# Kernel tuning notes

Measured on AMD Instinct MI355X. Metric: run time of the kernel, lower is better.

## Reference

```python
import jax, jax.numpy as jnp
import numpy as np

H, HKV, D, HID, INT = 16, 4, 128, 2048, 8192
ROPE_THETA = 10000.0
EPS = 1e-6
NEG = -1e30


def rmsnorm(x, w):
    v = jnp.mean(x * x, axis=-1, keepdims=True)
    return x * jax.lax.rsqrt(v + EPS) * w


def apply_rope(t, pos):
    # t: [B,S,h,D], pos: [S]
    half = D // 2
    inv_freq = 1.0 / (ROPE_THETA ** (jnp.arange(0, half, dtype=jnp.float32) / half))
    ang = pos.astype(jnp.float32)[:, None] * inv_freq  # [S, D/2]
    cos = jnp.cos(ang)[None, :, None, :]
    sin = jnp.sin(ang)[None, :, None, :]
    t1, t2 = t[..., :half], t[..., half:]
    return jnp.concatenate([t1 * cos - t2 * sin, t2 * cos + t1 * sin], axis=-1)


def setup_inputs() -> dict:
    key = jax.random.key(0)
    ks = jax.random.split(key, 5)
    B, S = 4, 1024
    s = 0.02  # init scale for weights
    return {
        "x": jax.random.normal(ks[0], (B, S, HID), jnp.float32),
        "ln1_w": jnp.ones((HID,), jnp.float32),
        "wqkv": jax.random.normal(ks[1], (HID, (H + 2 * HKV) * D), jnp.float32) * s,
        "wo": jax.random.normal(ks[2], (H * D, HID), jnp.float32) * s,
        "ln2_w": jnp.ones((HID,), jnp.float32),
        "w_gate_up": jax.random.normal(ks[3], (HID, 2 * INT), jnp.float32) * s,
        "w_down": jax.random.normal(ks[4], (INT, HID), jnp.float32) * s,
        "pos": jnp.arange(S, dtype=jnp.int32),
    }


def reference(x, ln1_w, wqkv, wo, ln2_w, w_gate_up, w_down, pos):
    B, S, _ = x.shape
    # --- attention block (prefill paged attention == dense causal attention) ---
    h = rmsnorm(x, ln1_w)
    qkv = h @ wqkv  # [B,S,(H+2*HKV)*D]
    q = qkv[..., : H * D].reshape(B, S, H, D)
    k = qkv[..., H * D : (H + HKV) * D].reshape(B, S, HKV, D)
    v = qkv[..., (H + HKV) * D :].reshape(B, S, HKV, D)
    q = apply_rope(q, pos)
    k = apply_rope(k, pos)
    g = H // HKV  # GQA group size
    k = jnp.repeat(k, g, axis=2)
    v = jnp.repeat(v, g, axis=2)
    scores = jnp.einsum("bqhd,bkhd->bhqk", q, k) / np.float32(np.sqrt(D))
    causal = pos[:, None] >= pos[None, :]  # [S,S]
    scores = jnp.where(causal[None, None], scores, NEG)
    attn = jax.nn.softmax(scores, axis=-1)
    o = jnp.einsum("bhqk,bkhd->bqhd", attn, v).reshape(B, S, H * D) @ wo
    h1 = x + o
    # --- SwiGLU MLP block ---
    gu = rmsnorm(h1, ln2_w) @ w_gate_up
    gate, up = gu[..., :INT], gu[..., INT:]
    return h1 + (jax.nn.silu(gate) * up) @ w_down
```

## Files before the change

kernel.cpp:

```cpp
#include <hip/hip_runtime.h>
#include <math.h>

#define B_    4
#define S_    1024
#define H_    16
#define HKV_  4
#define D_    128
#define HID_  2048
#define INT_  8192
#define QKVD_ 3072
#define NTOK_ 4096
#define NEG_  -1.0e30f

typedef unsigned short u16;
typedef unsigned int   u32;
typedef float  f32x4  __attribute__((ext_vector_type(4)));
typedef __bf16 bf16x8 __attribute__((ext_vector_type(8)));

__device__ __forceinline__ float bf2f(u16 v) {
    union { u32 u; float f; } c; c.u = ((u32)v) << 16; return c.f;
}
__device__ __forceinline__ u16 f2bf(float f) {
    union { float f; u32 u; } c; c.f = f;
    return (u16)((c.u + 0x7fffu + ((c.u >> 16) & 1u)) >> 16);
}

__device__ __forceinline__ void async_ld16(const u16* g, u16* l) {
    __builtin_amdgcn_global_load_lds(
        (const __attribute__((address_space(1))) void*)g,
        (__attribute__((address_space(3))) void*)l, 16, 0, 0);
}

__global__ void detect_k(const u16* __restrict__ w, int* __restrict__ flag) {
    if (threadIdx.x == 0) *flag = (w[0] == 0x3F80u) ? 0 : 1;
}

__global__ void cvt_x_k(const void* __restrict__ in, const int* __restrict__ flag,
                        u16* __restrict__ out) {
    int i = blockIdx.x * 256 + threadIdx.x;
    if (*flag == 0) {
        ((ushort4*)out)[i] = ((const ushort4*)in)[i];
    } else {
        float4 v = ((const float4*)in)[i];
        ushort4 o;
        o.x = f2bf(v.x); o.y = f2bf(v.y); o.z = f2bf(v.z); o.w = f2bf(v.w);
        ((ushort4*)out)[i] = o;
    }
}

__global__ void cvt_w_k(const void* __restrict__ in, const int* __restrict__ flag,
                        float* __restrict__ out, int n) {
    int i = blockIdx.x * 256 + threadIdx.x;
    if (i < n) out[i] = (*flag == 0) ? bf2f(((const u16*)in)[i]) : ((const float*)in)[i];
}

__global__ void transpose_k(const void* __restrict__ in, const int* __restrict__ flag,
                            u16* __restrict__ out, int K, int N) {
    __shared__ u16 t[64][65];
    const bool isf32 = (*flag != 0);
    int tx = blockIdx.x * 64;
    int ty = blockIdx.y * 64;
    const int c4 = (threadIdx.x & 15) * 4;
    const int r0 = threadIdx.x >> 4;
    for (int r = r0; r < 64; r += 16) {
        size_t idx = (size_t)(ty + r) * N + tx + c4;
        if (isf32) {
            float4 v = *(const float4*)((const float*)in + idx);
            t[c4 + 0][r] = f2bf(v.x); t[c4 + 1][r] = f2bf(v.y);
            t[c4 + 2][r] = f2bf(v.z); t[c4 + 3][r] = f2bf(v.w);
        } else {
            ushort4 v = *(const ushort4*)((const u16*)in + idx);
            t[c4 + 0][r] = v.x; t[c4 + 1][r] = v.y;
            t[c4 + 2][r] = v.z; t[c4 + 3][r] = v.w;
        }
    }
    __syncthreads();
    for (int i = threadIdx.x; i < 64 * 16; i += 256) {
        int r = i >> 4, c = (i & 15) * 4;
        ushort4 v;
        v.x = t[r][c]; v.y = t[r][c + 1]; v.z = t[r][c + 2]; v.w = t[r][c + 3];
        *(ushort4*)(out + (size_t)(tx + r) * K + ty + c) = v;
    }
}

__global__ void rmsnorm_k(const u16* __restrict__ x, const float* __restrict__ w,
                          u16* __restrict__ y) {
    int row = blockIdx.x;
    const u16* xr = x + (size_t)row * HID_;
    u16* yr = y + (size_t)row * HID_;
    int t = threadIdx.x;
    u16 xs[8];
    *(uint4*)xs = ((const uint4*)xr)[t];
    float v[8]; float ss = 0.f;
    #pragma unroll
    for (int i = 0; i < 8; i++) { v[i] = bf2f(xs[i]); ss += v[i] * v[i]; }
    #pragma unroll
    for (int o = 32; o > 0; o >>= 1) ss += __shfl_down(ss, o, 64);
    __shared__ float wsum[4];
    if ((t & 63) == 0) wsum[t >> 6] = ss;
    __syncthreads();
    float tot = wsum[0] + wsum[1] + wsum[2] + wsum[3];
    float scale = rsqrtf(tot * (1.0f / HID_) + 1e-6f);
    float4 w0 = ((const float4*)w)[t * 2];
    float4 w1 = ((const float4*)w)[t * 2 + 1];
    float wf[8] = {w0.x, w0.y, w0.z, w0.w, w1.x, w1.y, w1.z, w1.w};
    u16 ys[8];
    #pragma unroll
    for (int i = 0; i < 8; i++) ys[i] = f2bf(v[i] * scale * wf[i]);
    ((uint4*)yr)[t] = *(uint4*)ys;
}

__global__ void rope_table_k(const int* __restrict__ pos,
                             float* __restrict__ cosT, float* __restrict__ sinT) {
    int s = blockIdx.x;
    int d = threadIdx.x;
    double inv = exp(-((double)d / 64.0) * 9.210340371976184);
    double ang = (double)pos[s] * inv;
    cosT[s * 64 + d] = (float)cos(ang);
    sinT[s * 64 + d] = (float)sin(ang);
}

__global__ void rope_apply_k(u16* __restrict__ qkv, const float* __restrict__ cosT,
                             const float* __restrict__ sinT) {
    int id = blockIdx.x * 256 + threadIdx.x;
    int d4 = (id & 15) * 4;
    int rest = id >> 4;
    int head = rest % 20;
    int bs = rest / 20;
    int s = bs & (S_ - 1);
    size_t base = (size_t)bs * QKVD_ + head * D_;
    ushort4 lo = *(ushort4*)(qkv + base + d4);
    ushort4 hi = *(ushort4*)(qkv + base + 64 + d4);
    float4 c  = *(const float4*)(cosT + s * 64 + d4);
    float4 sn = *(const float4*)(sinT + s * 64 + d4);
    float t1[4] = {bf2f(lo.x), bf2f(lo.y), bf2f(lo.z), bf2f(lo.w)};
    float t2[4] = {bf2f(hi.x), bf2f(hi.y), bf2f(hi.z), bf2f(hi.w)};
    float cf[4] = {c.x, c.y, c.z, c.w};
    float sf[4] = {sn.x, sn.y, sn.z, sn.w};
    ushort4 olo, ohi;
    olo.x = f2bf(t1[0] * cf[0] - t2[0] * sf[0]);
    olo.y = f2bf(t1[1] * cf[1] - t2[1] * sf[1]);
    olo.z = f2bf(t1[2] * cf[2] - t2[2] * sf[2]);
    olo.w = f2bf(t1[3] * cf[3] - t2[3] * sf[3]);
    ohi.x = f2bf(t2[0] * cf[0] + t1[0] * sf[0]);
    ohi.y = f2bf(t2[1] * cf[1] + t1[1] * sf[1]);
    ohi.z = f2bf(t2[2] * cf[2] + t1[2] * sf[2]);
    ohi.w = f2bf(t2[3] * cf[3] + t1[3] * sf[3]);
    *(ushort4*)(qkv + base + d4)      = olo;
    *(ushort4*)(qkv + base + 64 + d4) = ohi;
}

template<int EPI>
__global__ __launch_bounds__(256) void gemm_bt_k(
    const u16* __restrict__ A, const u16* __restrict__ Bt,
    void* __restrict__ Cv, const u16* __restrict__ R,
    const int* __restrict__ flag, int M, int N, int K)
{
    __shared__ __align__(16) u16 As[128 * 32];
    __shared__ __align__(16) u16 Bs[128 * 32];

    int bx = blockIdx.x, by = blockIdx.y;
    {
        const int gx  = gridDim.x;
        const int nwg = gx * gridDim.y;
        const int orig = by * gx + bx;
        const int q = nwg >> 3, r = nwg & 7;
        const int xcd = orig & 7, loc = orig >> 3;
        const int wg = (xcd < r ? xcd * (q + 1) : r * (q + 1) + (xcd - r) * q) + loc;
        bx = wg % gx; by = wg / gx;
    }

    const int tid  = threadIdx.x;
    const int m0 = by * 128;
    const int n0 = bx * 128;
    const int wave = tid >> 6, lane = tid & 63;
    const int wm = (wave & 1) * 64, wn = (wave >> 1) * 64;
    const int r16 = lane & 15, quad = lane >> 4;

    const int f0 = tid * 8;
    const int f1 = f0 + 2048;
    const size_t arow0 = (size_t)(m0 + (f0 >> 5)) * K + (f0 & 31);
    const size_t arow1 = (size_t)(m0 + (f1 >> 5)) * K + (f1 & 31);
    const size_t brow0 = (size_t)(n0 + (f0 >> 5)) * K + (f0 & 31);
    const size_t brow1 = (size_t)(n0 + (f1 >> 5)) * K + (f1 & 31);

    f32x4 acc[4][4] = {};

    for (int k0 = 0; k0 < K; k0 += 32) {
        async_ld16(A  + arow0 + k0, As + f0);
        async_ld16(A  + arow1 + k0, As + f1);
        async_ld16(Bt + brow0 + k0, Bs + f0);
        async_ld16(Bt + brow1 + k0, Bs + f1);
        __syncthreads();
        bf16x8 a[4], b[4];
        #pragma unroll
        for (int i = 0; i < 4; i++)
            a[i] = *(const bf16x8*)(As + (wm + i * 16 + r16) * 32 + quad * 8);
        #pragma unroll
        for (int j = 0; j < 4; j++)
            b[j] = *(const bf16x8*)(Bs + (wn + j * 16 + r16) * 32 + quad * 8);
        #pragma unroll
        for (int i = 0; i < 4; i++)
            #pragma unroll
            for (int j = 0; j < 4; j++)
                acc[i][j] = __builtin_amdgcn_mfma_f32_16x16x32_bf16(a[i], b[j], acc[i][j], 0, 0, 0);
        __syncthreads();
    }

    u16* C16 = (u16*)Cv;
    float* C32 = (float*)Cv;
    bool f32out = false;
    if (EPI == 3) f32out = (*flag != 0);

    #pragma unroll
    for (int i = 0; i < 4; i++) {
        const int mb = m0 + wm + i * 16 + quad * 4;
        #pragma unroll
        for (int j = 0; j < 4; j++) {
            const int n = n0 + wn + j * 16 + r16;
            #pragma unroll
            for (int r = 0; r < 4; r++) {
                size_t idx = (size_t)(mb + r) * N + n;
                float v = acc[i][j][r];
                if (EPI == 1 || EPI == 3) v += bf2f(R[idx]);
                if (EPI == 3 && f32out) C32[idx] = v;
                else C16[idx] = f2bf(v);
            }
        }
    }
}

template<int EPI>
__global__ __launch_bounds__(512, 2) void gemm256_k(
    const u16* __restrict__ A, const u16* __restrict__ Bt,
    void* __restrict__ Cv, int M, int N, int K)
{
    __shared__ __align__(16) u16 lds[3 * 16384];

    int bx = blockIdx.x, by = blockIdx.y;
    {
        const int gx  = gridDim.x;
        const int nwg = gx * gridDim.y;
        const int orig = by * gx + bx;
        const int q = nwg >> 3, r = nwg & 7;
        const int xcd = orig & 7, loc = orig >> 3;
        const int wg = (xcd < r ? xcd * (q + 1) : r * (q + 1) + (xcd - r) * q) + loc;
        bx = wg % gx; by = wg / gx;
    }

    const int tid  = threadIdx.x;
    const int m0 = by * 256, n0 = bx * 256;
    const int wave = tid >> 6, lane = tid & 63;
    const int wmi = wave >> 2, wni = wave & 3;
    const int r16 = lane & 15, quad = lane >> 4;

    const int NT = K >> 5;

    auto stageA = [&](int bufi, int tt) {
        u16* dst = lds + bufi * 16384;
        const size_t gb = (size_t)m0 * K + (size_t)tt * 32;
        #pragma unroll
        for (int rr = 0; rr < 2; ++rr) {
            const int e = rr * 4096 + tid * 8;
            async_ld16(A + gb + (size_t)(e >> 5) * K + (e & 31), dst + e);
        }
    };
    auto stageB = [&](int bufi, int tt) {
        u16* dst = lds + bufi * 16384 + 8192;
        const size_t gb = (size_t)n0 * K + (size_t)tt * 32;
        #pragma unroll
        for (int rr = 0; rr < 2; ++rr) {
            const int e = rr * 4096 + tid * 8;
            async_ld16(Bt + gb + (size_t)(e >> 5) * K + (e & 31), dst + e);
        }
    };

    f32x4 acc[8][4] = {};

    stageA(0, 0); stageB(0, 0);
    stageA(1, 1); stageB(1, 1);
    asm volatile("s_waitcnt vmcnt(4)" ::: "memory");
    __builtin_amdgcn_s_barrier();

    const int aoff = wmi * 4096 + r16 * 32 + quad * 8;
    const int boff = 8192 + wni * 2048 + r16 * 32 + quad * 8;

    for (int t = 0; t < NT; ++t) {
        const u16* buf = lds + (t % 3) * 16384;
        const int nb = (t + 2) % 3;
        const bool pf = (t + 2) < NT;
        bf16x8 a[4], b[4], a2[4];
        #pragma unroll
        for (int i = 0; i < 4; ++i) a[i] = *(const bf16x8*)(buf + aoff + i * 512);
        #pragma unroll
        for (int j = 0; j < 4; ++j) b[j] = *(const bf16x8*)(buf + boff + j * 512);
        if (pf) stageA(nb, t + 2);
        __builtin_amdgcn_s_barrier();
        asm volatile("s_waitcnt lgkmcnt(0)" ::: "memory");
        __builtin_amdgcn_sched_barrier(0);
        __builtin_amdgcn_s_setprio(1);
        #pragma unroll
        for (int i = 0; i < 4; ++i)
            #pragma unroll
            for (int j = 0; j < 4; ++j)
                acc[i][j] = __builtin_amdgcn_mfma_f32_16x16x32_bf16(a[i], b[j], acc[i][j], 0, 0, 0);
        __builtin_amdgcn_s_setprio(0);
        __builtin_amdgcn_s_barrier();
        #pragma unroll
        for (int i = 0; i < 4; ++i) a2[i] = *(const bf16x8*)(buf + aoff + (i + 4) * 512);
        if (pf) stageB(nb, t + 2);
        __builtin_amdgcn_s_barrier();
        asm volatile("s_waitcnt lgkmcnt(0)" ::: "memory");
        __builtin_amdgcn_sched_barrier(0);
        __builtin_amdgcn_s_setprio(1);
        #pragma unroll
        for (int i = 0; i < 4; ++i)
            #pragma unroll
            for (int j = 0; j < 4; ++j)
                acc[i + 4][j] = __builtin_amdgcn_mfma_f32_16x16x32_bf16(a2[i], b[j], acc[i + 4][j], 0, 0, 0);
        __builtin_amdgcn_s_setprio(0);
        if (t == NT - 2) { asm volatile("s_waitcnt vmcnt(0)" ::: "memory"); }
        else             { asm volatile("s_waitcnt vmcnt(4)" ::: "memory"); }
        __builtin_amdgcn_s_barrier();
    }

    u16* C16 = (u16*)Cv;
    #pragma unroll
    for (int i = 0; i < 8; ++i) {
        const int mb = m0 + wmi * 128 + i * 16 + quad * 4;
        #pragma unroll
        for (int j = 0; j < 4; ++j) {
            const int n = n0 + wni * 64 + j * 16 + r16;
            #pragma unroll
            for (int r = 0; r < 4; ++r) {
                size_t idx = (size_t)(mb + r) * N + n;
                float v = acc[i][j][r];
                if (EPI == 2) { v = v / (1.f + __expf(-v)); v *= bf2f(C16[idx]); }
                C16[idx] = f2bf(v);
            }
        }
    }
}

__global__ __launch_bounds__(256) void attn_mfma_k(
    const u16* __restrict__ qkv, u16* __restrict__ out)
{
    __shared__ __align__(16) u16 Vt[128 * 136];
    __shared__ __align__(16) u16 Ps[64 * 136];

    int bswz_x, bswz_y, bswz_z;
    {
        const int orig = blockIdx.x + (S_ / 64) * (blockIdx.y + H_ * blockIdx.z);
        const int q = ((S_ / 64) * H_ * B_) >> 3;
        const int wg = (orig & 7) * q + (orig >> 3);
        bswz_x = wg & (S_ / 64 - 1);
        bswz_y = (wg >> 4) & (H_ - 1);
        bswz_z = wg >> 8;
    }

    const int tid  = threadIdx.x;
    const int wave = tid >> 6, lane = tid & 63;
    const int r16  = lane & 15, quad = lane >> 4;
    const int q0 = bswz_x * 64;
    const int h  = bswz_y;
    const int b  = bswz_z;
    const int kh = h >> 2;
    const float scale = 0.08838834764831845f;

    bf16x8 a_q[4];
    {
        const u16* qp = qkv + ((size_t)(b * S_ + q0 + wave * 16 + r16) * QKVD_ + h * D_ + quad * 8);
        #pragma unroll
        for (int ks = 0; ks < 4; ks++)
            a_q[ks] = *(const bf16x8*)(qp + ks * 32);
    }

    float mrun[4], lrun[4];
    #pragma unroll
    for (int r = 0; r < 4; r++) { mrun[r] = -3.0e38f; lrun[r] = 0.f; }
    f32x4 acc_o[8] = {};
    const int myrow_c = q0 + wave * 16 + quad * 4;

    const int ntiles = (q0 >> 7) + 1;
    for (int kt = 0; kt < ntiles; kt++) {
        const int j0 = kt * 128;
        __syncthreads();
        {
            const int key = tid & 127, dh = (tid >> 7) * 64;
            const u16* vp = qkv + ((size_t)(b * S_ + j0 + key) * QKVD_ + (H_ + HKV_ + kh) * D_ + dh);
            #pragma unroll
            for (int i = 0; i < 8; i++) {
                u16 tmp[8];
                *(uint4*)tmp = *(const uint4*)(vp + i * 8);
                #pragma unroll
                for (int j = 0; j < 8; j++)
                    Vt[(dh + i * 8 + j) * 136 + key] = tmp[j];
            }
        }
        f32x4 acc_s[8] = {};
        __builtin_amdgcn_s_setprio(1);
        #pragma unroll
        for (int ks = 0; ks < 4; ks++) {
            #pragma unroll
            for (int nt = 0; nt < 8; nt++) {
                const u16* kp = qkv + ((size_t)(b * S_ + j0 + nt * 16 + r16) * QKVD_
                                       + (H_ + kh) * D_ + ks * 32 + quad * 8);
                bf16x8 bk = *(const bf16x8*)kp;
                acc_s[nt] = __builtin_amdgcn_mfma_f32_16x16x32_bf16(a_q[ks], bk, acc_s[nt], 0, 0, 0);
            }
        }
        __builtin_amdgcn_s_setprio(0);
        const bool lastt = (kt == ntiles - 1);
        float mnew[4];
        #pragma unroll
        for (int r = 0; r < 4; r++) mnew[r] = mrun[r];
        #pragma unroll
        for (int nt = 0; nt < 8; nt++) {
            const int col = j0 + nt * 16 + r16;
            #pragma unroll
            for (int r = 0; r < 4; r++) {
                float v = acc_s[nt][r] * scale;
                if (lastt && col > myrow_c + r) v = NEG_;
                acc_s[nt][r] = v;
                mnew[r] = fmaxf(mnew[r], v);
            }
        }
        #pragma unroll
        for (int o = 1; o < 16; o <<= 1)
            #pragma unroll
            for (int r = 0; r < 4; r++)
                mnew[r] = fmaxf(mnew[r], __shfl_xor(mnew[r], o, 64));
        float alpha[4], lsum[4];
        #pragma unroll
        for (int r = 0; r < 4; r++) {
            alpha[r] = __expf(mrun[r] - mnew[r]);
            mrun[r] = mnew[r];
            lsum[r] = 0.f;
        }
        #pragma unroll
        for (int nt = 0; nt < 8; nt++) {
            #pragma unroll
            for (int r = 0; r < 4; r++) {
                float p = __expf(acc_s[nt][r] - mrun[r]);
                lsum[r] += p;
                Ps[(wave * 16 + quad * 4 + r) * 136 + nt * 16 + r16] = f2bf(p);
            }
        }
        #pragma unroll
        for (int o = 1; o < 16; o <<= 1)
            #pragma unroll
            for (int r = 0; r < 4; r++)
                lsum[r] += __shfl_xor(lsum[r], o, 64);
        #pragma unroll
        for (int r = 0; r < 4; r++) lrun[r] = lrun[r] * alpha[r] + lsum[r];
        #pragma unroll
        for (int nt = 0; nt < 8; nt++)
            #pragma unroll
            for (int r = 0; r < 4; r++) acc_o[nt][r] *= alpha[r];
        __syncthreads();
        __builtin_amdgcn_s_setprio(1);
        #pragma unroll
        for (int ks = 0; ks < 4; ks++) {
            bf16x8 ap = *(const bf16x8*)(Ps + (wave * 16 + r16) * 136 + ks * 32 + quad * 8);
            #pragma unroll
            for (int nt = 0; nt < 8; nt++) {
                bf16x8 bv = *(const bf16x8*)(Vt + (nt * 16 + r16) * 136 + ks * 32 + quad * 8);
                acc_o[nt] = __builtin_amdgcn_mfma_f32_16x16x32_bf16(ap, bv, acc_o[nt], 0, 0, 0);
            }
        }
        __builtin_amdgcn_s_setprio(0);
    }
    #pragma unroll
    for (int r = 0; r < 4; r++) {
        const float linv = 1.0f / lrun[r];
        const int tok = myrow_c + r;
        u16* orow = out + ((size_t)(b * S_ + tok) * (H_ * D_) + h * D_ + r16);
        #pragma unroll
        for (int nt = 0; nt < 8; nt++)
            orow[nt * 16] = f2bf(acc_o[nt][r] * linv);
    }
}

extern "C" void kernel_launch(void* const* d_in, const int* in_sizes, int n_in,
                              void* d_out, int out_size, void* d_ws, size_t ws_size,
                              hipStream_t stream)
{
    const void* x    = d_in[0];
    const u16*  ln1w = (const u16*)d_in[1];
    const void* wqkv = d_in[2];
    const void* wo   = d_in[3];
    const void* ln2w = d_in[4];
    const void* wgu  = d_in[5];
    const void* wd   = d_in[6];
    const int*  pos  = (const int*)d_in[7];

    char* wsb = (char*)d_ws;
    size_t off = 0;
    auto alloc = [&](size_t bytes) {
        char* p = wsb + off; off = (off + bytes + 255) & ~(size_t)255; return p;
    };
    int*  flag  = (int*)alloc(256);
    u16*  xb    = (u16*)alloc(2ull * NTOK_ * HID_);
    float* wln1 = (float*)alloc(4ull * HID_);
    float* wln2 = (float*)alloc(4ull * HID_);
    u16* wqkvT = (u16*)alloc(2ull * 3072 * 2048);
    u16* woT   = (u16*)alloc(2ull * 2048 * 2048);
    u16* wguT  = (u16*)alloc(2ull * 16384 * 2048);
    u16* wdT   = (u16*)alloc(2ull * 2048 * 8192);
    u16* h     = (u16*)alloc(2ull * NTOK_ * HID_);
    u16* qkv   = (u16*)alloc(2ull * NTOK_ * QKVD_);
    u16* h1    = (u16*)alloc(2ull * NTOK_ * HID_);
    u16* su    = (u16*)alloc(2ull * NTOK_ * INT_);
    float* cosT = (float*)alloc(4ull * S_ * 64);
    float* sinT = (float*)alloc(4ull * S_ * 64);
    u16* attn_out = h;
    u16* mlp_in   = qkv;

    detect_k<<<1, 64, 0, stream>>>(ln1w, flag);

    cvt_x_k<<<(NTOK_ * HID_ / 4 + 255) / 256, 256, 0, stream>>>(x, flag, xb);
    cvt_w_k<<<8, 256, 0, stream>>>(d_in[1], flag, wln1, HID_);
    cvt_w_k<<<8, 256, 0, stream>>>(ln2w, flag, wln2, HID_);

    transpose_k<<<dim3(3072 / 64, 2048 / 64), 256, 0, stream>>>(wqkv, flag, wqkvT, 2048, 3072);
    transpose_k<<<dim3(2048 / 64, 2048 / 64), 256, 0, stream>>>(wo, flag, woT, 2048, 2048);
    transpose_k<<<dim3(16384 / 64, 2048 / 64), 256, 0, stream>>>(wgu, flag, wguT, 2048, 16384);
    transpose_k<<<dim3(2048 / 64, 8192 / 64), 256, 0, stream>>>(wd, flag, wdT, 8192, 2048);

    rope_table_k<<<S_, 64, 0, stream>>>(pos, cosT, sinT);

    rmsnorm_k<<<NTOK_, 256, 0, stream>>>(xb, wln1, h);
    gemm256_k<0><<<dim3(3072 / 256, NTOK_ / 256), 512, 0, stream>>>(
        h, wqkvT, qkv, NTOK_, QKVD_, HID_);
    rope_apply_k<<<(NTOK_ * 20 * 16) / 256, 256, 0, stream>>>(qkv, cosT, sinT);
    attn_mfma_k<<<dim3(S_ / 64, H_, B_), 256, 0, stream>>>(qkv, attn_out);
    gemm_bt_k<1><<<dim3(2048 / 128, NTOK_ / 128), 256, 0, stream>>>(
        attn_out, woT, h1, xb, nullptr, NTOK_, HID_, HID_);
    rmsnorm_k<<<NTOK_, 256, 0, stream>>>(h1, wln2, mlp_in);
    gemm256_k<0><<<dim3(8192 / 256, NTOK_ / 256), 512, 0, stream>>>(
        mlp_in, wguT + (size_t)8192 * 2048, su, NTOK_, INT_, HID_);
    gemm256_k<2><<<dim3(8192 / 256, NTOK_ / 256), 512, 0, stream>>>(
        mlp_in, wguT, su, NTOK_, INT_, HID_);
    gemm_bt_k<3><<<dim3(2048 / 128, NTOK_ / 128), 256, 0, stream>>>(
        su, wdT, d_out, h1, flag, NTOK_, HID_, INT_);
}
```

Measured before the change: 1.150 ms.

## Replace residual GEMMs with pipelined 128x256 kernel and swizzle LDS tiles

The simple 128x128 gemm_bt_k used for the o-projection and down-projection becomes gemm_bt2_k, a 512-thread kernel with 128x256 tiles and a triple-buffered async-LDS pipeline modeled on gemm256_k. An XOR swizzle of the global column offset, matched by a permuted read offset, is added to both GEMMs to reduce LDS bank conflicts on the fragment reads. The aim is better latency hiding and higher MFMA use on the K=2048 and K=8192 residual GEMMs. The cost is a smaller grid (256 blocks for N=2048) and tighter register and LDS budgets, and the swizzle must index correctly.

```diff
diff --git a/kernel.cpp b/kernel.cpp
--- a/kernel.cpp
+++ b/kernel.cpp
@@ -29,6 +29,10 @@
     __builtin_amdgcn_global_load_lds(
         (const __attribute__((address_space(1))) void*)g,
         (__attribute__((address_space(3))) void*)l, 16, 0, 0);
+}
+
+__device__ __forceinline__ int swz_col(int e) {
+    return ((((e >> 3) & 3) ^ ((e >> 5) & 3) ^ ((e >> 7) & 3)) << 3);
 }
 
 __global__ void detect_k(const u16* __restrict__ w, int* __restrict__ flag) {
@@ -151,13 +155,11 @@
 }
 
 template<int EPI>
-__global__ __launch_bounds__(256) void gemm_bt_k(
+__global__ __launch_bounds__(512, 2) void gemm256_k(
     const u16* __restrict__ A, const u16* __restrict__ Bt,
-    void* __restrict__ Cv, const u16* __restrict__ R,
-    const int* __restrict__ flag, int M, int N, int K)
+    void* __restrict__ Cv, int M, int N, int K)
 {
-    __shared__ __align__(16) u16 As[128 * 32];
-    __shared__ __align__(16) u16 Bs[128 * 32];
+    __shared__ __align__(16) u16 lds[3 * 16384];
 
     int bx = blockIdx.x, by = blockIdx.y;
     {
@@ -171,71 +173,107 @@
     }
 
     const int tid  = threadIdx.x;
-    const int m0 = by * 128;
-    const int n0 = bx * 128;
+    const int m0 = by * 256, n0 = bx * 256;
     const int wave = tid >> 6, lane = tid & 63;
-    const int wm = (wave & 1) * 64, wn = (wave >> 1) * 64;
+    const int wmi = wave >> 2, wni = wave & 3;
     const int r16 = lane & 15, quad = lane >> 4;
 
-    const int f0 = tid * 8;
-    const int f1 = f0 + 2048;
-    const size_t arow0 = (size_t)(m0 + (f0 >> 5)) * K + (f0 & 31);
-    const size_t arow1 = (size_t)(m0 + (f1 >> 5)) * K + (f1 & 31);
-    const size_t brow0 = (size_t)(n0 + (f0 >> 5)) * K + (f0 & 31);
-    const size_t brow1 = (size_t)(n0 + (f1 >> 5)) * K + (f1 & 31);
-
-    f32x4 acc[4][4] = {};
-
-    for (int k0 = 0; k0 < K; k0 += 32) {
-        async_ld16(A  + arow0 + k0, As + f0);
-        async_ld16(A  + arow1 + k0, As + f1);
-        async_ld16(Bt + brow0 + k0, Bs + f0);
-        async_ld16(Bt + brow1 + k0, Bs + f1);
-        __syncthreads();
-        bf16x8 a[4], b[4];
-        #pragma unroll
-        for (int i = 0; i < 4; i++)
-            a[i] = *(const bf16x8*)(As + (wm + i * 16 + r16) * 32 + quad * 8);
-        #pragma unroll
-        for (int j = 0; j < 4; j++)
-            b[j] = *(const bf16x8*)(Bs + (wn + j * 16 + r16) * 32 + quad * 8);
-        #pragma unroll
-        for (int i = 0; i < 4; i++)
-            #pragma unroll
-            for (int j = 0; j < 4; j++)
+    const int NT = K >> 5;
+
+    auto stageA = [&](int bufi, int tt) {
+        u16* dst = lds + bufi * 16384;
+        const size_t gb = (size_t)m0 * K + (size_t)tt * 32;
+        #pragma unroll
+        for (int rr = 0; rr < 2; ++rr) {
+            const int e = rr * 4096 + tid * 8;
+            async_ld16(A + gb + (size_t)(e >> 5) * K + swz_col(e), dst + e);
+        }
+    };
+    auto stageB = [&](int bufi, int tt) {
+        u16* dst = lds + bufi * 16384 + 8192;
+        const size_t gb = (size_t)n0 * K + (size_t)tt * 32;
+        #pragma unroll
+        for (int rr = 0; rr < 2; ++rr) {
+            const int e = rr * 4096 + tid * 8;
+            async_ld16(Bt + gb + (size_t)(e >> 5) * K + swz_col(e), dst + e);
+        }
+    };
+
+    f32x4 acc[8][4] = {};
+
+    stageA(0, 0); stageB(0, 0);
+    stageA(1, 1); stageB(1, 1);
+    asm volatile("s_waitcnt vmcnt(4)" ::: "memory");
+    __builtin_amdgcn_s_barrier();
+
+    const int gsw = quad ^ (r16 & 3) ^ ((r16 >> 2) & 3);
+    const int aoff = wmi * 4096 + r16 * 32 + gsw * 8;
+    const int boff = 8192 + wni * 2048 + r16 * 32 + gsw * 8;
+
+    for (int t = 0; t < NT; ++t) {
+        const u16* buf = lds + (t % 3) * 16384;
+        const int nb = (t + 2) % 3;
+        const bool pf = (t + 2) < NT;
+        bf16x8 a[4], b[4], a2[4];
+        #pragma unroll
+        for (int i = 0; i < 4; ++i) a[i] = *(const bf16x8*)(buf + aoff + i * 512);
+        #pragma unroll
+        for (int j = 0; j < 4; ++j) b[j] = *(const bf16x8*)(buf + boff + j * 512);
+        if (pf) stageA(nb, t + 2);
+        __builtin_amdgcn_s_barrier();
+        asm volatile("s_waitcnt lgkmcnt(0)" ::: "memory");
+        __builtin_amdgcn_sched_barrier(0);
+        __builtin_amdgcn_s_setprio(1);
+        #pragma unroll
+        for (int i = 0; i < 4; ++i)
+            #pragma unroll
+            for (int j = 0; j < 4; ++j)
                 acc[i][j] = __builtin_amdgcn_mfma_f32_16x16x32_bf16(a[i], b[j], acc[i][j], 0, 0, 0);
-        __syncthreads();
+        __builtin_amdgcn_s_setprio(0);
+        __builtin_amdgcn_s_barrier();
+        #pragma unroll
+        for (int i = 0; i < 4; ++i) a2[i] = *(const bf16x8*)(buf + aoff + (i + 4) * 512);
+        if (pf) stageB(nb, t + 2);
+        __builtin_amdgcn_s_barrier();
+        asm volatile("s_waitcnt lgkmcnt(0)" ::: "memory");
+        __builtin_amdgcn_sched_barrier(0);
+        __builtin_amdgcn_s_setprio(1);
+        #pragma unroll
+        for (int i = 0; i < 4; ++i)
+            #pragma unroll
+            for (int j = 0; j < 4; ++j)
+                acc[i + 4][j] = __builtin_amdgcn_mfma_f32_16x16x32_bf16(a2[i], b[j], acc[i + 4][j], 0, 0, 0);
+        __builtin_amdgcn_s_setprio(0);
+        if (t == NT - 2) { asm volatile("s_waitcnt vmcnt(0)" ::: "memory"); }
+        else             { asm volatile("s_waitcnt vmcnt(4)" ::: "memory"); }
+        __builtin_amdgcn_s_barrier();
     }
 
     u16* C16 = (u16*)Cv;
-    float* C32 = (float*)Cv;
-    bool f32out = false;
-    if (EPI == 3) f32out = (*flag != 0);
-
-    #pragma unroll
-    for (int i = 0; i < 4; i++) {
-        const int mb = m0 + wm + i * 16 + quad * 4;
-        #pragma unroll
-        for (int j = 0; j < 4; j++) {
-            const int n = n0 + wn + j * 16 + r16;
-            #pragma unroll
-            for (int r = 0; r < 4; r++) {
+    #pragma unroll
+    for (int i = 0; i < 8; ++i) {
+        const int mb = m0 + wmi * 128 + i * 16 + quad * 4;
+        #pragma unroll
+        for (int j = 0; j < 4; ++j) {
+            const int n = n0 + wni * 64 + j * 16 + r16;
+            #pragma unroll
+            for (int r = 0; r < 4; ++r) {
                 size_t idx = (size_t)(mb + r) * N + n;
                 float v = acc[i][j][r];
-                if (EPI == 1 || EPI == 3) v += bf2f(R[idx]);
-                if (EPI == 3 && f32out) C32[idx] = v;
-                else C16[idx] = f2bf(v);
+                if (EPI == 2) { v = v / (1.f + __expf(-v)); v *= bf2f(C16[idx]); }
+                C16[idx] = f2bf(v);
             }
         }
     }
 }
 
 template<int EPI>
-__global__ __launch_bounds__(512, 2) void gemm256_k(
+__global__ __launch_bounds__(512, 2) void gemm_bt2_k(
     const u16* __restrict__ A, const u16* __restrict__ Bt,
-    void* __restrict__ Cv, int M, int N, int K)
+    void* __restrict__ Cv, const u16* __restrict__ R,
+    const int* __restrict__ flag, int M, int N, int K)
 {
-    __shared__ __align__(16) u16 lds[3 * 16384];
+    __shared__ __align__(16) u16 lds[3 * 12288];
 
     int bx = blockIdx.x, by = blockIdx.y;
     {
@@ -249,7 +287,7 @@
     }
 
     const int tid  = threadIdx.x;
-    const int m0 = by * 256, n0 = bx * 256;
+    const int m0 = by * 128, n0 = bx * 256;
     const int wave = tid >> 6, lane = tid & 63;
     const int wmi = wave >> 2, wni = wave & 3;
     const int r16 = lane & 15, quad = lane >> 4;
@@ -257,43 +295,41 @@
     const int NT = K >> 5;
 
     auto stageA = [&](int bufi, int tt) {
-        u16* dst = lds + bufi * 16384;
+        u16* dst = lds + bufi * 12288;
         const size_t gb = (size_t)m0 * K + (size_t)tt * 32;
+        const int e = tid * 8;
+        async_ld16(A + gb + (size_t)(e >> 5) * K + swz_col(e), dst + e);
+    };
+    auto stageB = [&](int bufi, int tt) {
+        u16* dst = lds + bufi * 12288 + 4096;
+        const size_t gb = (size_t)n0 * K + (size_t)tt * 32;
         #pragma unroll
         for (int rr = 0; rr < 2; ++rr) {
             const int e = rr * 4096 + tid * 8;
-            async_ld16(A + gb + (size_t)(e >> 5) * K + (e & 31), dst + e);
+            async_ld16(Bt + gb + (size_t)(e >> 5) * K + swz_col(e), dst + e);
         }
     };
-    auto stageB = [&](int bufi, int tt) {
-        u16* dst = lds + bufi * 16384 + 8192;
-        const size_t gb = (size_t)n0 * K + (size_t)tt * 32;
-        #pragma unroll
-        for (int rr = 0; rr < 2; ++rr) {
-            const int e = rr * 4096 + tid * 8;
-            async_ld16(Bt + gb + (size_t)(e >> 5) * K + (e & 31), dst + e);
-        }
-    };
-
-    f32x4 acc[8][4] = {};
+
+    f32x4 acc[4][4] = {};
 
     stageA(0, 0); stageB(0, 0);
     stageA(1, 1); stageB(1, 1);
-    asm volatile("s_waitcnt vmcnt(4)" ::: "memory");
+    asm volatile("s_waitcnt vmcnt(3)" ::: "memory");
     __builtin_amdgcn_s_barrier();
 
-    const int aoff = wmi * 4096 + r16 * 32 + quad * 8;
-    const int boff = 8192 + wni * 2048 + r16 * 32 + quad * 8;
+    const int gsw = quad ^ (r16 & 3) ^ ((r16 >> 2) & 3);
+    const int aoff = wmi * 2048 + r16 * 32 + gsw * 8;
+    const int boff = 4096 + wni * 2048 + r16 * 32 + gsw * 8;
 
     for (int t = 0; t < NT; ++t) {
-        const u16* buf = lds + (t % 3) * 16384;
+        const u16* buf = lds + (t % 3) * 12288;
         const int nb = (t + 2) % 3;
         const bool pf = (t + 2) < NT;
-        bf16x8 a[4], b[4], a2[4];
+        bf16x8 a[4], b2[2], b3[2];
         #pragma unroll
         for (int i = 0; i < 4; ++i) a[i] = *(const bf16x8*)(buf + aoff + i * 512);
         #pragma unroll
-        for (int j = 0; j < 4; ++j) b[j] = *(const bf16x8*)(buf + boff + j * 512);
+        for (int j = 0; j < 2; ++j) b2[j] = *(const bf16x8*)(buf + boff + j * 512);
         if (pf) stageA(nb, t + 2);
         __builtin_amdgcn_s_barrier();
         asm volatile("s_waitcnt lgkmcnt(0)" ::: "memory");
@@ -302,12 +338,12 @@
         #pragma unroll
         for (int i = 0; i < 4; ++i)
             #pragma unroll
-            for (int j = 0; j < 4; ++j)
-                acc[i][j] = __builtin_amdgcn_mfma_f32_16x16x32_bf16(a[i], b[j], acc[i][j], 0, 0, 0);
+            for (int j = 0; j < 2; ++j)
+                acc[i][j] = __builtin_amdgcn_mfma_f32_16x16x32_bf16(a[i], b2[j], acc[i][j], 0, 0, 0);
         __builtin_amdgcn_s_setprio(0);
         __builtin_amdgcn_s_barrier();
         #pragma unroll
-        for (int i = 0; i < 4; ++i) a2[i] = *(const bf16x8*)(buf + aoff + (i + 4) * 512);
+        for (int j = 0; j < 2; ++j) b3[j] = *(const bf16x8*)(buf + boff + (j + 2) * 512);
         if (pf) stageB(nb, t + 2);
         __builtin_amdgcn_s_barrier();
         asm volatile("s_waitcnt lgkmcnt(0)" ::: "memory");
@@ -316,18 +352,22 @@
         #pragma unroll
         for (int i = 0; i < 4; ++i)
             #pragma unroll
-            for (int j = 0; j < 4; ++j)
-                acc[i + 4][j] = __builtin_amdgcn_mfma_f32_16x16x32_bf16(a2[i], b[j], acc[i + 4][j], 0, 0, 0);
+            for (int j = 0; j < 2; ++j)
+                acc[i][j + 2] = __builtin_amdgcn_mfma_f32_16x16x32_bf16(a[i], b3[j], acc[i][j + 2], 0, 0, 0);
         __builtin_amdgcn_s_setprio(0);
         if (t == NT - 2) { asm volatile("s_waitcnt vmcnt(0)" ::: "memory"); }
-        else             { asm volatile("s_waitcnt vmcnt(4)" ::: "memory"); }
+        else             { asm volatile("s_waitcnt vmcnt(3)" ::: "memory"); }
         __builtin_amdgcn_s_barrier();
     }
 
     u16* C16 = (u16*)Cv;
-    #pragma unroll
-    for (int i = 0; i < 8; ++i) {
-        const int mb = m0 + wmi * 128 + i * 16 + quad * 4;
+    float* C32 = (float*)Cv;
+    bool f32out = false;
+    if (EPI == 3) f32out = (*flag != 0);
+
+    #pragma unroll
+    for (int i = 0; i < 4; ++i) {
+        const int mb = m0 + wmi * 64 + i * 16 + quad * 4;
         #pragma unroll
         for (int j = 0; j < 4; ++j) {
             const int n = n0 + wni * 64 + j * 16 + r16;
@@ -335,8 +375,9 @@
             for (int r = 0; r < 4; ++r) {
                 size_t idx = (size_t)(mb + r) * N + n;
                 float v = acc[i][j][r];
-                if (EPI == 2) { v = v / (1.f + __expf(-v)); v *= bf2f(C16[idx]); }
-                C16[idx] = f2bf(v);
+                v += bf2f(R[idx]);
+                if (EPI == 3 && f32out) C32[idx] = v;
+                else C16[idx] = f2bf(v);
             }
         }
     }
@@ -534,13 +575,13 @@
         h, wqkvT, qkv, NTOK_, QKVD_, HID_);
     rope_apply_k<<<(NTOK_ * 20 * 16) / 256, 256, 0, stream>>>(qkv, cosT, sinT);
     attn_mfma_k<<<dim3(S_ / 64, H_, B_), 256, 0, stream>>>(qkv, attn_out);
-    gemm_bt_k<1><<<dim3(2048 / 128, NTOK_ / 128), 256, 0, stream>>>(
+    gemm_bt2_k<1><<<dim3(2048 / 256, NTOK_ / 128), 512, 0, stream>>>(
         attn_out, woT, h1, xb, nullptr, NTOK_, HID_, HID_);
     rmsnorm_k<<<NTOK_, 256, 0, stream>>>(h1, wln2, mlp_in);
     gemm256_k<0><<<dim3(8192 / 256, NTOK_ / 256), 512, 0, stream>>>(
         mlp_in, wguT + (size_t)8192 * 2048, su, NTOK_, INT_, HID_);
     gemm256_k<2><<<dim3(8192 / 256, NTOK_ / 256), 512, 0, stream>>>(
         mlp_in, wguT, su, NTOK_, INT_, HID_);
-    gemm_bt_k<3><<<dim3(2048 / 128, NTOK_ / 128), 256, 0, stream>>>(
+    gemm_bt2_k<3><<<dim3(2048 / 256, NTOK_ / 128), 512, 0, stream>>>(
         su, wdT, d_out, h1, flag, NTOK_, HID_, INT_);
 }
```

Measured after the change: 1.093 ms. -4.9%, faster.
